# Optimization experiments

Measured on AMD Instinct MI355X. Metric: run time of the kernel, lower is better.

## Reference

```python
import jax, jax.numpy as jnp
import numpy as np
from jax import lax

D = 2
SIGMA = 2.0
K = 9
CH = 64
PAD = (K - 1) // 2  # rel_padding=0 default -> padding = half kernel
STRIDE = 1


def make_gaussian_filter(sigma, k, channels):
    # separable Gaussian -> full 2D kernel, normalized to sum 1 (same math as torch grid version)
    mean = (k - 1) / 2.0
    c = jnp.arange(k, dtype=jnp.float32) - mean
    g1 = jnp.exp(-(c ** 2) / (2.0 * sigma ** 2))
    f = g1[:, None] * g1[None, :]          # [k,k]; exp(-(dx^2+dy^2)/2s^2)
    f = f / jnp.sum(f)
    return jnp.broadcast_to(f[None, None], (channels, 1, k, k))  # OIHW depthwise


def setup_inputs() -> dict:
    key = jax.random.key(0)
    x = jax.random.normal(key, (16, CH, 256, 256), dtype=jnp.float32)
    filt = make_gaussian_filter(SIGMA, K, CH)
    return {"x": x, "filt": filt}


def _blur(x, filt, groups):
    return lax.conv_general_dilated(
        x, filt,
        window_strides=(STRIDE, STRIDE),
        padding=[(PAD, PAD), (PAD, PAD)],
        dimension_numbers=("NCHW", "OIHW", "NCHW"),
        feature_group_count=groups,
    )


def reference(x, filt):
    y = _blur(x, filt, CH)  # depthwise blur, [N,C,H,W]
    # edge-correction weights: blur of ones (all channel filters are identical,
    # so a single-channel conv suffices and broadcasts over C)
    ones = jnp.ones((1, 1) + x.shape[2:], dtype=x.dtype)
    w = _blur(ones, filt[:1], 1)  # [1,1,H,W]
    return y / w
```

## Files before the change

### kernel.cpp

```cpp
#include <hip/hip_runtime.h>


#define HH 256
#define WW 256
#define W4 (WW / 4)
#define STRIPS 4
#define SROWS (HH / STRIPS)

#define G0 0.02763055f
#define G1 0.06628225f
#define G2 0.12383154f
#define G3 0.18017382f
#define G4 0.20416361f

typedef float f4 __attribute__((ext_vector_type(4)));

__device__ __forceinline__ f4 shfl4(f4 v, int src) {
    f4 r;
    r.x = __shfl(v.x, src, 64);
    r.y = __shfl(v.y, src, 64);
    r.z = __shfl(v.z, src, 64);
    r.w = __shfl(v.w, src, 64);
    return r;
}

__global__ __launch_bounds__(256) void gauss_blur_kernel(
    const float* __restrict__ x, float* __restrict__ out)
{
    const float G[9] = {G0, G1, G2, G3, G4, G3, G2, G1, G0};

    const int plane = blockIdx.x;
    const int wid   = threadIdx.x >> 6;
    const int lane  = threadIdx.x & 63;
    const f4* __restrict__ src = (const f4*)(x + (size_t)plane * (HH * WW));
    f4* __restrict__ dst       = (f4*)(out + (size_t)plane * (HH * WW));
    const int r0   = wid * SROWS;
    const int rmax = (r0 + SROWS + 4 < HH) ? (r0 + SROWS + 4) : HH;

    f4 inv_wx = (f4){1.f, 1.f, 1.f, 1.f};
    if (lane == 0 || lane == 63) {
        float w[4];
        #pragma unroll
        for (int j = 0; j < 4; ++j) {
            const int c = lane * 4 + j;
            float s = 0.f;
            #pragma unroll
            for (int i = 0; i < 9; ++i) {
                const int q = c + i - 4;
                if (q >= 0 && q < WW) s += G[i];
            }
            w[j] = 1.f / s;
        }
        inv_wx = (f4){w[0], w[1], w[2], w[3]};
    }

    auto ldrow = [&](int r) -> f4 {
        return ((unsigned)r < (unsigned)rmax) ? src[r * W4 + lane]
                                              : (f4){0.f, 0.f, 0.f, 0.f};
    };

    f4 win[9];
    #pragma unroll
    for (int i = 0; i < 9; ++i) win[i] = ldrow(r0 + i - 4);

    auto step = [&](int r, f4 nxt) {
        f4 v = G[0] * win[0];
        #pragma unroll
        for (int i = 1; i < 9; ++i) {
            v.x = fmaf(G[i], win[i].x, v.x);
            v.y = fmaf(G[i], win[i].y, v.y);
            v.z = fmaf(G[i], win[i].z, v.z);
            v.w = fmaf(G[i], win[i].w, v.w);
        }
        f4 vm = shfl4(v, lane - 1);
        f4 vp = shfl4(v, lane + 1);
        if (lane == 0)  vm = (f4){0.f, 0.f, 0.f, 0.f};
        if (lane == 63) vp = (f4){0.f, 0.f, 0.f, 0.f};
        const float s[12] = {vm.x, vm.y, vm.z, vm.w,
                             v.x,  v.y,  v.z,  v.w,
                             vp.x, vp.y, vp.z, vp.w};
        float o[4];
        #pragma unroll
        for (int j = 0; j < 4; ++j) {
            float a = G[0] * s[j];
            #pragma unroll
            for (int i = 1; i < 9; ++i) a = fmaf(G[i], s[j + i], a);
            o[j] = a;
        }
        float iwy = 1.f;
        if (r < 4 || r >= HH - 4) {
            float wy = 0.f;
            #pragma unroll
            for (int i = 0; i < 9; ++i) {
                const int q = r + i - 4;
                if (q >= 0 && q < HH) wy += G[i];
            }
            iwy = 1.f / wy;
        }
        f4 res = (f4){o[0] * inv_wx.x * iwy, o[1] * inv_wx.y * iwy,
                      o[2] * inv_wx.z * iwy, o[3] * inv_wx.w * iwy};
        __builtin_nontemporal_store(res, &dst[r * W4 + lane]);
        #pragma unroll
        for (int i = 0; i < 8; ++i) win[i] = win[i + 1];
        win[8] = nxt;
    };

    f4 pa0 = ldrow(r0 + 5), pa1 = ldrow(r0 + 6), pa2 = ldrow(r0 + 7), pa3 = ldrow(r0 + 8);

    for (int rr = 0; rr < SROWS; rr += 8) {
        const int r = r0 + rr;
        f4 pb0 = ldrow(r + 9),  pb1 = ldrow(r + 10), pb2 = ldrow(r + 11), pb3 = ldrow(r + 12);
        step(r,     pa0);
        step(r + 1, pa1);
        step(r + 2, pa2);
        step(r + 3, pa3);
        pa0 = ldrow(r + 13); pa1 = ldrow(r + 14); pa2 = ldrow(r + 15); pa3 = ldrow(r + 16);
        step(r + 4, pb0);
        step(r + 5, pb1);
        step(r + 6, pb2);
        step(r + 7, pb3);
    }
}

extern "C" void kernel_launch(void* const* d_in, const int* in_sizes, int n_in,
                              void* d_out, int out_size, void* d_ws, size_t ws_size,
                              hipStream_t stream)
{
    const float* x = (const float*)d_in[0];
    float* out = (float*)d_out;
    const int nplanes = in_sizes[0] / (HH * WW);
    gauss_blur_kernel<<<nplanes, 256, 0, stream>>>(x, out);
}
```

Baseline: 99.34 us.

## Halve strips per plane and deepen row prefetch pipeline

Each plane is now split into 2 row strips instead of 4, so each block runs 128 threads, and the halo rows loaded twice per plane drop from 3 pairs to 1. Row loads are prefetched 8-16 rows ahead instead of 4-8, and the four results of each group are stored together after computing. The aim is more memory-level parallelism and fewer redundant halo reads. The cost is more live registers, and with only 1024 planes the kernel now has 1024 blocks of 2 waves each, which may lower occupancy.

```diff
diff --git a/kernel.cpp b/kernel.cpp
--- a/kernel.cpp
+++ b/kernel.cpp
@@ -4,7 +4,7 @@
 #define HH 256
 #define WW 256
 #define W4 (WW / 4)
-#define STRIPS 4
+#define STRIPS 2
 #define SROWS (HH / STRIPS)
 
 #define G0 0.02763055f
@@ -24,7 +24,7 @@
     return r;
 }
 
-__global__ __launch_bounds__(256) void gauss_blur_kernel(
+__global__ __launch_bounds__(128) void gauss_blur_kernel(
     const float* __restrict__ x, float* __restrict__ out)
 {
     const float G[9] = {G0, G1, G2, G3, G4, G3, G2, G1, G0};
@@ -63,7 +63,7 @@
     #pragma unroll
     for (int i = 0; i < 9; ++i) win[i] = ldrow(r0 + i - 4);
 
-    auto step = [&](int r, f4 nxt) {
+    auto step = [&](int r, f4 nxt) -> f4 {
         f4 v = G[0] * win[0];
         #pragma unroll
         for (int i = 1; i < 9; ++i) {
@@ -97,28 +97,40 @@
             }
             iwy = 1.f / wy;
         }
-        f4 res = (f4){o[0] * inv_wx.x * iwy, o[1] * inv_wx.y * iwy,
-                      o[2] * inv_wx.z * iwy, o[3] * inv_wx.w * iwy};
-        __builtin_nontemporal_store(res, &dst[r * W4 + lane]);
         #pragma unroll
         for (int i = 0; i < 8; ++i) win[i] = win[i + 1];
         win[8] = nxt;
+        return (f4){o[0] * inv_wx.x * iwy, o[1] * inv_wx.y * iwy,
+                    o[2] * inv_wx.z * iwy, o[3] * inv_wx.w * iwy};
     };
 
-    f4 pa0 = ldrow(r0 + 5), pa1 = ldrow(r0 + 6), pa2 = ldrow(r0 + 7), pa3 = ldrow(r0 + 8);
+    f4 a0 = ldrow(r0 + 5),  a1 = ldrow(r0 + 6),  a2 = ldrow(r0 + 7),  a3 = ldrow(r0 + 8);
+    f4 b0 = ldrow(r0 + 9),  b1 = ldrow(r0 + 10), b2 = ldrow(r0 + 11), b3 = ldrow(r0 + 12);
+    f4 c0 = ldrow(r0 + 13), c1 = ldrow(r0 + 14), c2 = ldrow(r0 + 15), c3 = ldrow(r0 + 16);
 
     for (int rr = 0; rr < SROWS; rr += 8) {
         const int r = r0 + rr;
-        f4 pb0 = ldrow(r + 9),  pb1 = ldrow(r + 10), pb2 = ldrow(r + 11), pb3 = ldrow(r + 12);
-        step(r,     pa0);
-        step(r + 1, pa1);
-        step(r + 2, pa2);
-        step(r + 3, pa3);
-        pa0 = ldrow(r + 13); pa1 = ldrow(r + 14); pa2 = ldrow(r + 15); pa3 = ldrow(r + 16);
-        step(r + 4, pb0);
-        step(r + 5, pb1);
-        step(r + 6, pb2);
-        step(r + 7, pb3);
+        f4 t0 = ldrow(r + 17), t1 = ldrow(r + 18), t2 = ldrow(r + 19), t3 = ldrow(r + 20);
+        f4 o0 = step(r,     a0);
+        f4 o1 = step(r + 1, a1);
+        f4 o2 = step(r + 2, a2);
+        f4 o3 = step(r + 3, a3);
+        __builtin_nontemporal_store(o0, &dst[(r    ) * W4 + lane]);
+        __builtin_nontemporal_store(o1, &dst[(r + 1) * W4 + lane]);
+        __builtin_nontemporal_store(o2, &dst[(r + 2) * W4 + lane]);
+        __builtin_nontemporal_store(o3, &dst[(r + 3) * W4 + lane]);
+        f4 u0 = ldrow(r + 21), u1 = ldrow(r + 22), u2 = ldrow(r + 23), u3 = ldrow(r + 24);
+        o0 = step(r + 4, b0);
+        o1 = step(r + 5, b1);
+        o2 = step(r + 6, b2);
+        o3 = step(r + 7, b3);
+        __builtin_nontemporal_store(o0, &dst[(r + 4) * W4 + lane]);
+        __builtin_nontemporal_store(o1, &dst[(r + 5) * W4 + lane]);
+        __builtin_nontemporal_store(o2, &dst[(r + 6) * W4 + lane]);
+        __builtin_nontemporal_store(o3, &dst[(r + 7) * W4 + lane]);
+        a0 = c0; a1 = c1; a2 = c2; a3 = c3;
+        b0 = t0; b1 = t1; b2 = t2; b3 = t3;
+        c0 = u0; c1 = u1; c2 = u2; c3 = u3;
     }
 }
 
@@ -129,5 +141,5 @@
     const float* x = (const float*)d_in[0];
     float* out = (float*)d_out;
     const int nplanes = in_sizes[0] / (HH * WW);
-    gauss_blur_kernel<<<nplanes, 256, 0, stream>>>(x, out);
+    gauss_blur_kernel<<<nplanes, 128, 0, stream>>>(x, out);
 }
```

Result: faster. 88.24 us (-11.2%).
